# Performance work log

Measured on AMD Instinct MI355X. Metric: run time of the kernel, lower is better.

## Reference

```python
import jax, jax.numpy as jnp
import numpy as np

N_NODES = 100_000
N_EDGES = 3_200_000
IN_CH = 128
HID = 128


def setup_inputs() -> dict:
    key = jax.random.key(0)
    k1, k2, k3, k4, k5 = jax.random.split(key, 5)
    x = jax.random.normal(k1, (N_NODES, IN_CH), dtype=jnp.float32)
    edge_index = jax.random.randint(k2, (2, N_EDGES), 0, N_NODES, dtype=jnp.int64)
    # GCNConv params: glorot-style weights, zero bias (as in PyG defaults)
    s1 = 1.0 / np.sqrt(IN_CH)
    s2 = 1.0 / np.sqrt(HID)
    W1 = jax.random.uniform(k3, (IN_CH, HID), jnp.float32, -s1, s1)
    b1 = jnp.zeros((HID,), jnp.float32)
    W2 = jax.random.uniform(k4, (HID, HID), jnp.float32, -s2, s2)
    b2 = jnp.zeros((HID,), jnp.float32)
    return {"x": x, "edge_index": edge_index, "W1": W1, "b1": b1, "W2": W2, "b2": b2}


def _gcn_conv(x, src, dst, W, b):
    """PyG GCNConv: add self-loops, symmetric D^-1/2 (A+I) D^-1/2 norm,
    linear transform first, then aggregate, then bias."""
    n = x.shape[0]
    loops = jnp.arange(n, dtype=src.dtype)
    s = jnp.concatenate([src, loops])          # [E+N]
    d = jnp.concatenate([dst, loops])          # [E+N]
    w = jnp.ones(s.shape[0], dtype=x.dtype)    # edge_weight=None -> ones
    deg = jax.ops.segment_sum(w, d, num_segments=n)            # [N]
    dinv = jnp.where(deg > 0, jax.lax.rsqrt(deg), 0.0)         # deg^-1/2
    norm = dinv[s] * w * dinv[d]                                # [E+N]
    xw = x @ W                                                  # [N, H]
    msg = xw[s] * norm[:, None]                                 # [E+N, H] gather
    out = jax.ops.segment_sum(msg, d, num_segments=n)           # [N, H] scatter
    return out + b


def reference(x, edge_index, W1, b1, W2, b2):
    src, dst = edge_index[0], edge_index[1]
    h1 = jax.nn.relu(_gcn_conv(x, src, dst, W1, b1))
    h2 = jax.nn.relu(_gcn_conv(h1, src, dst, W2, b2))
    return jnp.concatenate([h1, h2], axis=1)   # [N, 2*HID]
```

## Files before the change

kernel.cpp:

```cpp
#include <hip/hip_runtime.h>
#include <hip/hip_bf16.h>
#include <stdint.h>

#define NN 100000
#define BSH 9
#define BSZ 512
#define NBUCK 196
#define CAP 24576

typedef float vfloat4 __attribute__((ext_vector_type(4)));

static __device__ __forceinline__ float bf_lo(unsigned int u) {
    union { unsigned int i; float f; } c; c.i = u << 16; return c.f;
}
static __device__ __forceinline__ float bf_hi(unsigned int u) {
    union { unsigned int i; float f; } c; c.i = u & 0xffff0000u; return c.f;
}
static __device__ __forceinline__ unsigned short f2bf(float f) {
    union { float f; unsigned int i; } c; c.f = f;
    unsigned int r = (c.i + 0x7fffu + ((c.i >> 16) & 1u)) >> 16;
    return (unsigned short)r;
}

__global__ void k_init(int* __restrict__ gcursor, unsigned int* __restrict__ xwb_row_nn) {
    int i = threadIdx.x;
    if (i < NBUCK) gcursor[i] = i * CAP;
    if (i < 64) xwb_row_nn[i] = 0u;
}

__global__ __launch_bounds__(256) void k_bucket(const int* __restrict__ eb, int E,
                                                int* __restrict__ gcursor,
                                                unsigned int* __restrict__ pairs) {
    __shared__ int hist[NBUCK];
    __shared__ int gbase[NBUCK];
    __shared__ int shflag;
    int t = threadIdx.x;
    if (t < 64) {
        int v = eb[2 * t + 1];
        unsigned long long m = __ballot(v == 0);
        if (t == 0) shflag = (m == ~0ull) ? 1 : 0;
    }
    for (int i = t; i < NBUCK; i += 256) hist[i] = 0;
    __syncthreads();
    int sh = shflag;
    size_t base = (size_t)blockIdx.x * 4096;
    int srcs[16], rank[16], bks[16], dls[16];
#pragma unroll
    for (int k = 0; k < 16; k++) {
        size_t e = base + (size_t)k * 256 + t;
        if (e < (size_t)E) {
            int s = eb[e << sh];
            int d = eb[((size_t)E + e) << sh];
            int b = d >> BSH;
            srcs[k] = s; bks[k] = b; dls[k] = d & (BSZ - 1);
            rank[k] = atomicAdd(&hist[b], 1);
        } else {
            bks[k] = -1;
        }
    }
    __syncthreads();
    for (int i = t; i < NBUCK; i += 256) {
        int c = hist[i];
        gbase[i] = (c > 0) ? atomicAdd(&gcursor[i], c) : 0;
    }
    __syncthreads();
#pragma unroll
    for (int k = 0; k < 16; k++) {
        if (bks[k] >= 0) {
            int pos = gbase[bks[k]] + rank[k];
            if (pos < (bks[k] + 1) * CAP)
                pairs[pos] = ((unsigned int)dls[k] << 17) | (unsigned int)srcs[k];
        }
    }
}

__global__ __launch_bounds__(1024) void k_pass2(const unsigned int* __restrict__ pairs,
                                                const int* __restrict__ gcursor,
                                                int* __restrict__ csr, int* __restrict__ ptr,
                                                int* __restrict__ degv, float* __restrict__ dinv) {
    __shared__ int hist2[BSZ * 8];
    __shared__ int cur2[BSZ * 8];
    __shared__ int hist[BSZ];
    __shared__ int lofs[BSZ];
    __shared__ int scanw[BSZ];
    __shared__ int lcsr[CAP];
    int b = blockIdx.x, t = threadIdx.x;
    int base = b * CAP;
    int cnt = gcursor[b] - base;
    if (cnt > CAP) cnt = CAP;
    for (int i = t; i < BSZ * 8; i += 1024) hist2[i] = 0;
    __syncthreads();
    for (int i = t; i < cnt; i += 1024) {
        unsigned int p = pairs[base + i];
        int key = (int)((p >> 17) << 3) | (int)((p & 0x1FFFFu) >> 14);
        atomicAdd(&hist2[key], 1);
    }
    __syncthreads();
    int h = 0;
    if (t < BSZ) {
#pragma unroll
        for (int oc = 0; oc < 8; oc++) h += hist2[(t << 3) | oc];
        scanw[t] = h;
        hist[t] = h;
    }
    __syncthreads();
    for (int d = 1; d < BSZ; d <<= 1) {
        int x = 0;
        if (t < BSZ && t >= d) x = scanw[t - d];
        __syncthreads();
        if (t < BSZ) scanw[t] += x;
        __syncthreads();
    }
    if (t < BSZ) {
        int excl = scanw[t] - h;
        lofs[t] = excl;
        int run = excl;
#pragma unroll
        for (int oc = 0; oc < 8; oc++) { cur2[(t << 3) | oc] = run; run += hist2[(t << 3) | oc]; }
    }
    __syncthreads();
    for (int i = t; i < cnt; i += 1024) {
        unsigned int p = pairs[base + i];
        int src = (int)(p & 0x1FFFFu);
        int key = (int)((p >> 17) << 3) | (src >> 14);
        int pos = atomicAdd(&cur2[key], 1);
        lcsr[pos] = src;
    }
    __syncthreads();
    for (int i = t; i < cnt; i += 1024) csr[base + i] = lcsr[i];
    int n0 = b << BSH;
    if (t < BSZ) {
        int n = n0 + t;
        if (n < NN) {
            int dg = hist[t];
            degv[n] = dg;
            ptr[n] = base + lofs[t];
            dinv[n] = rsqrtf((float)(dg + 1));
        }
    }
}

__global__ __launch_bounds__(256) void k_gemm(const float* __restrict__ A, int lda,
                                              const float* __restrict__ W,
                                              const float* __restrict__ dinv,
                                              unsigned short* __restrict__ outb, int M) {
    __shared__ float Wl[32 * 128];
    __shared__ float Al[64 * 33];
    int t = threadIdx.x;
    int row0 = blockIdx.x * 64;
    int cg = t & 15, rg = t >> 4;
    int c0 = cg * 8, r0 = rg * 4;
    float acc[4][8];
#pragma unroll
    for (int i = 0; i < 4; i++)
#pragma unroll
        for (int j = 0; j < 8; j++) acc[i][j] = 0.f;

    for (int kb = 0; kb < 4; kb++) {
        __syncthreads();
        const float4* Wg = (const float4*)(W + kb * 32 * 128);
        float4* Wl4 = (float4*)Wl;
#pragma unroll
        for (int i = 0; i < 4; i++) Wl4[t + 256 * i] = Wg[t + 256 * i];
#pragma unroll
        for (int i = 0; i < 2; i++) {
            int idx = t + 256 * i;
            int r = idx >> 3, c4 = idx & 7;
            int grow = row0 + r;
            float4 v = make_float4(0.f, 0.f, 0.f, 0.f);
            if (grow < M) v = *(const float4*)(A + (size_t)grow * lda + kb * 32 + c4 * 4);
            float* dp = &Al[r * 33 + c4 * 4];
            dp[0] = v.x; dp[1] = v.y; dp[2] = v.z; dp[3] = v.w;
        }
        __syncthreads();
#pragma unroll 8
        for (int k = 0; k < 32; k++) {
            float wv[8];
            *(float4*)&wv[0] = *(const float4*)&Wl[k * 128 + c0];
            *(float4*)&wv[4] = *(const float4*)&Wl[k * 128 + c0 + 4];
            float av[4];
#pragma unroll
            for (int i = 0; i < 4; i++) av[i] = Al[(r0 + i) * 33 + k];
#pragma unroll
            for (int i = 0; i < 4; i++)
#pragma unroll
                for (int j = 0; j < 8; j++)
                    acc[i][j] = fmaf(av[i], wv[j], acc[i][j]);
        }
    }
#pragma unroll
    for (int i = 0; i < 4; i++) {
        int grow = row0 + r0 + i;
        if (grow < M) {
            float dv = dinv[grow];
            unsigned int w[4];
#pragma unroll
            for (int j = 0; j < 4; j++)
                w[j] = (unsigned int)f2bf(acc[i][2 * j] * dv) |
                       ((unsigned int)f2bf(acc[i][2 * j + 1] * dv) << 16);
            uint4 pk = make_uint4(w[0], w[1], w[2], w[3]);
            *(uint4*)(outb + (size_t)grow * 128 + c0) = pk;
        }
    }
}

__global__ __launch_bounds__(256) void k_aggr(const unsigned short* __restrict__ xwb,
                                              const int* __restrict__ csr, const int* __restrict__ ptr,
                                              const int* __restrict__ degv,
                                              const float* __restrict__ dinv, const float* __restrict__ bias,
                                              float* __restrict__ outf, int N) {
    int wid = (blockIdx.x * 256 + threadIdx.x) >> 6;
    int lane = threadIdx.x & 63;
    if (wid >= N) return;
    int n = wid;
    int g  = lane >> 4;
    int sl = lane & 15;
    int st = ptr[n];
    int en = st + degv[n];
    const uint4* xq = (const uint4*)xwb + sl;
    float acc[8] = {0.f, 0.f, 0.f, 0.f, 0.f, 0.f, 0.f, 0.f};
    for (int j = st; j < en; j += 64) {
        int e = j + lane;
        int sp = (e < en) ? csr[e] : NN;
        int cnt = en - j; if (cnt > 64) cnt = 64;
        int cntr = (cnt + 7) & ~7;
        for (int q = 0; q < cntr; q += 8) {
            int s0 = __shfl(sp, q + g);
            int s1 = __shfl(sp, q + 4 + g);
            uint4 u0 = xq[(size_t)s0 * 16];
            uint4 u1 = xq[(size_t)s1 * 16];
            acc[0] += bf_lo(u0.x); acc[1] += bf_hi(u0.x);
            acc[2] += bf_lo(u0.y); acc[3] += bf_hi(u0.y);
            acc[4] += bf_lo(u0.z); acc[5] += bf_hi(u0.z);
            acc[6] += bf_lo(u0.w); acc[7] += bf_hi(u0.w);
            acc[0] += bf_lo(u1.x); acc[1] += bf_hi(u1.x);
            acc[2] += bf_lo(u1.y); acc[3] += bf_hi(u1.y);
            acc[4] += bf_lo(u1.z); acc[5] += bf_hi(u1.z);
            acc[6] += bf_lo(u1.w); acc[7] += bf_hi(u1.w);
        }
    }
    if (g == 0) {
        uint4 u = xq[(size_t)n * 16];
        acc[0] += bf_lo(u.x); acc[1] += bf_hi(u.x);
        acc[2] += bf_lo(u.y); acc[3] += bf_hi(u.y);
        acc[4] += bf_lo(u.z); acc[5] += bf_hi(u.z);
        acc[6] += bf_lo(u.w); acc[7] += bf_hi(u.w);
    }
#pragma unroll
    for (int i = 0; i < 8; i++) {
        acc[i] += __shfl_xor(acc[i], 16);
        acc[i] += __shfl_xor(acc[i], 32);
    }
    if (g == 0) {
        float dn = dinv[n];
        const float4* bq = (const float4*)bias + 2 * sl;
        float4 b0 = bq[0], b1 = bq[1];
        vfloat4 o0, o1;
        o0.x = fmaxf(fmaf(acc[0], dn, b0.x), 0.f);
        o0.y = fmaxf(fmaf(acc[1], dn, b0.y), 0.f);
        o0.z = fmaxf(fmaf(acc[2], dn, b0.z), 0.f);
        o0.w = fmaxf(fmaf(acc[3], dn, b0.w), 0.f);
        o1.x = fmaxf(fmaf(acc[4], dn, b1.x), 0.f);
        o1.y = fmaxf(fmaf(acc[5], dn, b1.y), 0.f);
        o1.z = fmaxf(fmaf(acc[6], dn, b1.z), 0.f);
        o1.w = fmaxf(fmaf(acc[7], dn, b1.w), 0.f);
        vfloat4* op = (vfloat4*)(outf + (size_t)n * 256 + sl * 8);
        __builtin_nontemporal_store(o0, op);
        __builtin_nontemporal_store(o1, op + 1);
    }
}

extern "C" void kernel_launch(void* const* d_in, const int* in_sizes, int n_in,
                              void* d_out, int out_size, void* d_ws, size_t ws_size,
                              hipStream_t stream) {
    const float* x  = (const float*)d_in[0];
    const int*   eb = (const int*)d_in[1];
    const float* W1 = (const float*)d_in[2];
    const float* b1 = (const float*)d_in[3];
    const float* W2 = (const float*)d_in[4];
    const float* b2 = (const float*)d_in[5];
    float* out = (float*)d_out;

    int E = in_sizes[1] / 2;

    char* w = (char*)d_ws;
    size_t o = 0;
    auto carve = [&](size_t bytes) { char* p = w + o; o += (bytes + 255) & ~(size_t)255; return p; };
    int*   gcursor = (int*)carve((size_t)NBUCK * 4);
    int*   ptr     = (int*)carve((size_t)NN * 4);
    int*   deg     = (int*)carve((size_t)NN * 4);
    float* dinv    = (float*)carve((size_t)NN * 4);
    int*   csr     = (int*)carve((size_t)NBUCK * CAP * 4);
    size_t big = (size_t)(NN + 1) * 128 * 2;
    size_t pb  = (size_t)NBUCK * CAP * 4;
    char* shared_region = carve(big > pb ? big : pb);
    unsigned int*   pairs = (unsigned int*)shared_region;
    unsigned short* xwb   = (unsigned short*)shared_region;
    (void)ws_size;

    int EB4 = (E + 4095) / 4096;
    int GB  = (NN + 63) / 64;
    int AB  = (NN + 3) / 4;

    k_init<<<1, 256, 0, stream>>>(gcursor, (unsigned int*)(xwb + (size_t)NN * 128));
    k_bucket<<<EB4, 256, 0, stream>>>(eb, E, gcursor, pairs);
    k_pass2<<<NBUCK, 1024, 0, stream>>>(pairs, gcursor, csr, ptr, deg, dinv);

    k_gemm<<<GB, 256, 0, stream>>>(x, 128, W1, dinv, xwb, NN);
    k_aggr<<<AB, 256, 0, stream>>>(xwb, csr, ptr, deg, dinv, b1, out, NN);

    k_gemm<<<GB, 256, 0, stream>>>(out, 256, W2, dinv, xwb, NN);
    k_aggr<<<AB, 256, 0, stream>>>(xwb, csr, ptr, deg, dinv, b2, out + 128, NN);
}
```

Measured before the change: 513.3 us.

## Quantize transformed features to per-row int8 with scales for aggregation gather

The GEMM epilogue now quantizes each dinv-scaled output row to unsigned 8-bit values with an offset of 128 and one float scale per row, replacing bf16 storage. The aggregation kernel gathers 128-byte rows plus a per-source scale. It uses 8 lanes per row and 16 accumulators per lane, and subtracts the offset with a summed-scale correction term. This halves the random-gather traffic that dominates the edge aggregation, at the cost of extra scalar scale loads, more conversion ALU work and reduced numeric precision.

```diff
diff --git a/kernel.cpp b/kernel.cpp
--- a/kernel.cpp
+++ b/kernel.cpp
@@ -10,22 +10,10 @@
 
 typedef float vfloat4 __attribute__((ext_vector_type(4)));
 
-static __device__ __forceinline__ float bf_lo(unsigned int u) {
-    union { unsigned int i; float f; } c; c.i = u << 16; return c.f;
-}
-static __device__ __forceinline__ float bf_hi(unsigned int u) {
-    union { unsigned int i; float f; } c; c.i = u & 0xffff0000u; return c.f;
-}
-static __device__ __forceinline__ unsigned short f2bf(float f) {
-    union { float f; unsigned int i; } c; c.f = f;
-    unsigned int r = (c.i + 0x7fffu + ((c.i >> 16) & 1u)) >> 16;
-    return (unsigned short)r;
-}
-
-__global__ void k_init(int* __restrict__ gcursor, unsigned int* __restrict__ xwb_row_nn) {
+__global__ void k_init(int* __restrict__ gcursor, float* __restrict__ scalev) {
     int i = threadIdx.x;
     if (i < NBUCK) gcursor[i] = i * CAP;
-    if (i < 64) xwb_row_nn[i] = 0u;
+    if (i == 0) scalev[NN] = 0.f;
 }
 
 __global__ __launch_bounds__(256) void k_bucket(const int* __restrict__ eb, int E,
@@ -143,7 +131,8 @@
 __global__ __launch_bounds__(256) void k_gemm(const float* __restrict__ A, int lda,
                                               const float* __restrict__ W,
                                               const float* __restrict__ dinv,
-                                              unsigned short* __restrict__ outb, int M) {
+                                              unsigned char* __restrict__ qb,
+                                              float* __restrict__ scalev, int M) {
     __shared__ float Wl[32 * 128];
     __shared__ float Al[64 * 33];
     int t = threadIdx.x;
@@ -188,23 +177,42 @@
                     acc[i][j] = fmaf(av[i], wv[j], acc[i][j]);
         }
     }
+    float am[4];
+#pragma unroll
+    for (int i = 0; i < 4; i++) {
+        int grow = row0 + r0 + i;
+        float dv = (grow < M) ? dinv[grow] : 0.f;
+        float m = 0.f;
+#pragma unroll
+        for (int j = 0; j < 8; j++) { acc[i][j] *= dv; m = fmaxf(m, fabsf(acc[i][j])); }
+        am[i] = m;
+    }
+#pragma unroll
+    for (int mask = 1; mask <= 8; mask <<= 1) {
+#pragma unroll
+        for (int i = 0; i < 4; i++) am[i] = fmaxf(am[i], __shfl_xor(am[i], mask));
+    }
 #pragma unroll
     for (int i = 0; i < 4; i++) {
         int grow = row0 + r0 + i;
         if (grow < M) {
-            float dv = dinv[grow];
-            unsigned int w[4];
-#pragma unroll
-            for (int j = 0; j < 4; j++)
-                w[j] = (unsigned int)f2bf(acc[i][2 * j] * dv) |
-                       ((unsigned int)f2bf(acc[i][2 * j + 1] * dv) << 16);
-            uint4 pk = make_uint4(w[0], w[1], w[2], w[3]);
-            *(uint4*)(outb + (size_t)grow * 128 + c0) = pk;
-        }
-    }
-}
-
-__global__ __launch_bounds__(256) void k_aggr(const unsigned short* __restrict__ xwb,
+            float rs = (am[i] > 0.f) ? (127.f / am[i]) : 0.f;
+            unsigned int lo = 0, hi = 0;
+#pragma unroll
+            for (int j = 0; j < 4; j++) lo |= ((unsigned int)(fmaf(acc[i][j], rs, 128.5f))) << (8 * j);
+#pragma unroll
+            for (int j = 0; j < 4; j++) hi |= ((unsigned int)(fmaf(acc[i][4 + j], rs, 128.5f))) << (8 * j);
+            *(uint2*)(qb + (size_t)grow * 128 + cg * 8) = make_uint2(lo, hi);
+        }
+    }
+    if (cg < 4) {
+        int grow = row0 + r0 + cg;
+        if (grow < M) scalev[grow] = am[cg] * (1.f / 127.f);
+    }
+}
+
+__global__ __launch_bounds__(256) void k_aggr(const unsigned char* __restrict__ qb,
+                                              const float* __restrict__ scalev,
                                               const int* __restrict__ csr, const int* __restrict__ ptr,
                                               const int* __restrict__ degv,
                                               const float* __restrict__ dinv, const float* __restrict__ bias,
@@ -213,60 +221,79 @@
     int lane = threadIdx.x & 63;
     if (wid >= N) return;
     int n = wid;
-    int g  = lane >> 4;
-    int sl = lane & 15;
+    int g  = lane >> 3;
+    int sl = lane & 7;
     int st = ptr[n];
     int en = st + degv[n];
-    const uint4* xq = (const uint4*)xwb + sl;
-    float acc[8] = {0.f, 0.f, 0.f, 0.f, 0.f, 0.f, 0.f, 0.f};
+    const uint4* xq = (const uint4*)qb + sl;
+    float acc[16];
+#pragma unroll
+    for (int i = 0; i < 16; i++) acc[i] = 0.f;
+    float ksum = 0.f;
+
+#define ACC16(u, sc)                                                          \
+    acc[0]  = fmaf((float)( (u).x        & 0xffu), sc, acc[0]);               \
+    acc[1]  = fmaf((float)(((u).x >>  8) & 0xffu), sc, acc[1]);               \
+    acc[2]  = fmaf((float)(((u).x >> 16) & 0xffu), sc, acc[2]);               \
+    acc[3]  = fmaf((float)( (u).x >> 24         ), sc, acc[3]);               \
+    acc[4]  = fmaf((float)( (u).y        & 0xffu), sc, acc[4]);               \
+    acc[5]  = fmaf((float)(((u).y >>  8) & 0xffu), sc, acc[5]);               \
+    acc[6]  = fmaf((float)(((u).y >> 16) & 0xffu), sc, acc[6]);               \
+    acc[7]  = fmaf((float)( (u).y >> 24         ), sc, acc[7]);               \
+    acc[8]  = fmaf((float)( (u).z        & 0xffu), sc, acc[8]);               \
+    acc[9]  = fmaf((float)(((u).z >>  8) & 0xffu), sc, acc[9]);               \
+    acc[10] = fmaf((float)(((u).z >> 16) & 0xffu), sc, acc[10]);              \
+    acc[11] = fmaf((float)( (u).z >> 24         ), sc, acc[11]);              \
+    acc[12] = fmaf((float)( (u).w        & 0xffu), sc, acc[12]);              \
+    acc[13] = fmaf((float)(((u).w >>  8) & 0xffu), sc, acc[13]);              \
+    acc[14] = fmaf((float)(((u).w >> 16) & 0xffu), sc, acc[14]);              \
+    acc[15] = fmaf((float)( (u).w >> 24         ), sc, acc[15]);
+
     for (int j = st; j < en; j += 64) {
         int e = j + lane;
         int sp = (e < en) ? csr[e] : NN;
         int cnt = en - j; if (cnt > 64) cnt = 64;
         int cntr = (cnt + 7) & ~7;
         for (int q = 0; q < cntr; q += 8) {
-            int s0 = __shfl(sp, q + g);
-            int s1 = __shfl(sp, q + 4 + g);
-            uint4 u0 = xq[(size_t)s0 * 16];
-            uint4 u1 = xq[(size_t)s1 * 16];
-            acc[0] += bf_lo(u0.x); acc[1] += bf_hi(u0.x);
-            acc[2] += bf_lo(u0.y); acc[3] += bf_hi(u0.y);
-            acc[4] += bf_lo(u0.z); acc[5] += bf_hi(u0.z);
-            acc[6] += bf_lo(u0.w); acc[7] += bf_hi(u0.w);
-            acc[0] += bf_lo(u1.x); acc[1] += bf_hi(u1.x);
-            acc[2] += bf_lo(u1.y); acc[3] += bf_hi(u1.y);
-            acc[4] += bf_lo(u1.z); acc[5] += bf_hi(u1.z);
-            acc[6] += bf_lo(u1.w); acc[7] += bf_hi(u1.w);
+            int s = __shfl(sp, q + g);
+            uint4 u = xq[(size_t)s * 8];
+            float sc = scalev[s];
+            ksum += sc;
+            ACC16(u, sc)
         }
     }
     if (g == 0) {
-        uint4 u = xq[(size_t)n * 16];
-        acc[0] += bf_lo(u.x); acc[1] += bf_hi(u.x);
-        acc[2] += bf_lo(u.y); acc[3] += bf_hi(u.y);
-        acc[4] += bf_lo(u.z); acc[5] += bf_hi(u.z);
-        acc[6] += bf_lo(u.w); acc[7] += bf_hi(u.w);
-    }
-#pragma unroll
-    for (int i = 0; i < 8; i++) {
+        uint4 u = xq[(size_t)n * 8];
+        float sc = scalev[n];
+        ksum += sc;
+        ACC16(u, sc)
+    }
+#undef ACC16
+#pragma unroll
+    for (int i = 0; i < 16; i++) {
+        acc[i] += __shfl_xor(acc[i], 8);
         acc[i] += __shfl_xor(acc[i], 16);
         acc[i] += __shfl_xor(acc[i], 32);
     }
+    ksum += __shfl_xor(ksum, 8);
+    ksum += __shfl_xor(ksum, 16);
+    ksum += __shfl_xor(ksum, 32);
+
     if (g == 0) {
         float dn = dinv[n];
-        const float4* bq = (const float4*)bias + 2 * sl;
-        float4 b0 = bq[0], b1 = bq[1];
-        vfloat4 o0, o1;
-        o0.x = fmaxf(fmaf(acc[0], dn, b0.x), 0.f);
-        o0.y = fmaxf(fmaf(acc[1], dn, b0.y), 0.f);
-        o0.z = fmaxf(fmaf(acc[2], dn, b0.z), 0.f);
-        o0.w = fmaxf(fmaf(acc[3], dn, b0.w), 0.f);
-        o1.x = fmaxf(fmaf(acc[4], dn, b1.x), 0.f);
-        o1.y = fmaxf(fmaf(acc[5], dn, b1.y), 0.f);
-        o1.z = fmaxf(fmaf(acc[6], dn, b1.z), 0.f);
-        o1.w = fmaxf(fmaf(acc[7], dn, b1.w), 0.f);
-        vfloat4* op = (vfloat4*)(outf + (size_t)n * 256 + sl * 8);
-        __builtin_nontemporal_store(o0, op);
-        __builtin_nontemporal_store(o1, op + 1);
+        float corr = -128.f * dn * ksum;
+        const float4* bq = (const float4*)(bias + 16 * sl);
+        float* op = outf + (size_t)n * 256 + 16 * sl;
+#pragma unroll
+        for (int v4 = 0; v4 < 4; v4++) {
+            float4 bb = bq[v4];
+            vfloat4 o;
+            o.x = fmaxf(fmaf(dn, acc[4 * v4 + 0], corr + bb.x), 0.f);
+            o.y = fmaxf(fmaf(dn, acc[4 * v4 + 1], corr + bb.y), 0.f);
+            o.z = fmaxf(fmaf(dn, acc[4 * v4 + 2], corr + bb.z), 0.f);
+            o.w = fmaxf(fmaf(dn, acc[4 * v4 + 3], corr + bb.w), 0.f);
+            __builtin_nontemporal_store(o, (vfloat4*)op + v4);
+        }
     }
 }
 
@@ -290,25 +317,26 @@
     int*   ptr     = (int*)carve((size_t)NN * 4);
     int*   deg     = (int*)carve((size_t)NN * 4);
     float* dinv    = (float*)carve((size_t)NN * 4);
+    float* scalev  = (float*)carve((size_t)(NN + 1) * 4);
     int*   csr     = (int*)carve((size_t)NBUCK * CAP * 4);
-    size_t big = (size_t)(NN + 1) * 128 * 2;
+    size_t qbb = (size_t)(NN + 1) * 128;
     size_t pb  = (size_t)NBUCK * CAP * 4;
-    char* shared_region = carve(big > pb ? big : pb);
-    unsigned int*   pairs = (unsigned int*)shared_region;
-    unsigned short* xwb   = (unsigned short*)shared_region;
+    char* shared_region = carve(qbb > pb ? qbb : pb);
+    unsigned int*  pairs = (unsigned int*)shared_region;
+    unsigned char* qb    = (unsigned char*)shared_region;
     (void)ws_size;
 
     int EB4 = (E + 4095) / 4096;
     int GB  = (NN + 63) / 64;
     int AB  = (NN + 3) / 4;
 
-    k_init<<<1, 256, 0, stream>>>(gcursor, (unsigned int*)(xwb + (size_t)NN * 128));
+    k_init<<<1, 256, 0, stream>>>(gcursor, scalev);
     k_bucket<<<EB4, 256, 0, stream>>>(eb, E, gcursor, pairs);
     k_pass2<<<NBUCK, 1024, 0, stream>>>(pairs, gcursor, csr, ptr, deg, dinv);
 
-    k_gemm<<<GB, 256, 0, stream>>>(x, 128, W1, dinv, xwb, NN);
-    k_aggr<<<AB, 256, 0, stream>>>(xwb, csr, ptr, deg, dinv, b1, out, NN);
-
-    k_gemm<<<GB, 256, 0, stream>>>(out, 256, W2, dinv, xwb, NN);
-    k_aggr<<<AB, 256, 0, stream>>>(xwb, csr, ptr, deg, dinv, b2, out + 128, NN);
-}
+    k_gemm<<<GB, 256, 0, stream>>>(x, 128, W1, dinv, qb, scalev, NN);
+    k_aggr<<<AB, 256, 0, stream>>>(qb, scalev, csr, ptr, deg, dinv, b1, out, NN);
+
+    k_gemm<<<GB, 256, 0, stream>>>(out, 256, W2, dinv, qb, scalev, NN);
+    k_aggr<<<AB, 256, 0, stream>>>(qb, scalev, csr, ptr, deg, dinv, b2, out + 128, NN);
+}
```

New measurement: 461.5 us. 1.11x faster.
